# Kernel optimization log

Hardware: AMD Instinct MI355X
Metric: run time of the kernel (lower is better)

Reference implementation:

```python
import jax
import jax.numpy as jnp
from jax import lax
import numpy as np

B, T, D = 64, 256, 512      # batch, seq_len, input_size
H, P, L = 1024, 256, 4      # hidden_size, proj_size, num_layers


def setup_inputs() -> dict:
    key = jax.random.key(0)
    ks = jax.random.split(key, 12)
    s = 1.0 / np.sqrt(H)
    inp = {
        "x": jax.random.normal(ks[0], (B, T, D), dtype=jnp.float32),
        # layer 0 (input dim D)
        "W_ih0": jax.random.uniform(ks[1], (4 * H, D), minval=-s, maxval=s, dtype=jnp.float32),
        "W_hh0": jax.random.uniform(ks[2], (4 * H, P), minval=-s, maxval=s, dtype=jnp.float32),
        "b_ih0": jax.random.uniform(ks[3], (4 * H,), minval=-s, maxval=s, dtype=jnp.float32),
        "b_hh0": jax.random.uniform(ks[4], (4 * H,), minval=-s, maxval=s, dtype=jnp.float32),
        "W_hr0": jax.random.uniform(ks[5], (P, H), minval=-s, maxval=s, dtype=jnp.float32),
        # layers 1..L-1 (input dim P), stacked
        "W_ihs": jax.random.uniform(ks[6], (L - 1, 4 * H, P), minval=-s, maxval=s, dtype=jnp.float32),
        "W_hhs": jax.random.uniform(ks[7], (L - 1, 4 * H, P), minval=-s, maxval=s, dtype=jnp.float32),
        "b_ihs": jax.random.uniform(ks[8], (L - 1, 4 * H), minval=-s, maxval=s, dtype=jnp.float32),
        "b_hhs": jax.random.uniform(ks[9], (L - 1, 4 * H), minval=-s, maxval=s, dtype=jnp.float32),
        "W_hrs": jax.random.uniform(ks[10], (L - 1, P, H), minval=-s, maxval=s, dtype=jnp.float32),
    }
    return inp


def _lstm_proj_layer(x, W_ih, W_hh, b_ih, b_hh, W_hr):
    """One projected-LSTM layer (PyTorch gate order i,f,g,o). x: [B,T,Din] -> [B,T,P]."""
    b, t, _ = x.shape
    p, h = W_hr.shape
    # precompute input contribution to gates: [T,B,4H]
    xg = jnp.swapaxes(jnp.einsum('btd,gd->btg', x, W_ih) + b_ih + b_hh, 0, 1)

    def step(carry, g_in):
        hp, c = carry                      # hp: [B,P] projected hidden, c: [B,H]
        g = g_in + hp @ W_hh.T             # [B,4H]
        i, f, gg, o = jnp.split(g, 4, axis=-1)
        i = jax.nn.sigmoid(i)
        f = jax.nn.sigmoid(f)
        gg = jnp.tanh(gg)
        o = jax.nn.sigmoid(o)
        c = f * c + i * gg
        hp = (o * jnp.tanh(c)) @ W_hr.T    # projection: [B,P]
        return (hp, c), hp

    init = (jnp.zeros((b, p), x.dtype), jnp.zeros((b, h), x.dtype))
    _, hs = lax.scan(step, init, xg)       # hs: [T,B,P]
    return jnp.swapaxes(hs, 0, 1)


def reference(x, W_ih0, W_hh0, b_ih0, b_hh0, W_hr0, W_ihs, W_hhs, b_ihs, b_hhs, W_hrs):
    y = _lstm_proj_layer(x, W_ih0, W_hh0, b_ih0, b_hh0, W_hr0)
    for l in range(L - 1):  # fixed small layer count
        y = _lstm_proj_layer(y, W_ihs[l], W_hhs[l], b_ihs[l], b_hhs[l], W_hrs[l])
    return y[:, -1, :]  # [B, P] last-timestep output, as in forward()
```

## Files before the change

kernel.cpp:

```cpp
#include <hip/hip_runtime.h>
#include <cstdint>
#include <cstddef>


#define B_ 64
#define T_ 256
#define D_ 512
#define H_ 1024
#define P_ 256
#define NWG 256
#define NTHR 512

using short8  = __attribute__((ext_vector_type(8))) short;
using f32x16  = __attribute__((ext_vector_type(16))) float;
using f32x4   = __attribute__((ext_vector_type(4))) float;

__device__ inline float bf2f(short s) {
  unsigned u = ((unsigned)(unsigned short)s) << 16;
  return __builtin_bit_cast(float, u);
}
__device__ inline unsigned short f2bf(float f) {
  unsigned u = __builtin_bit_cast(unsigned, f);
  u += 0x7fffu + ((u >> 16) & 1u);
  return (unsigned short)(u >> 16);
}
__device__ inline void split1(float v, short& hi, short& lo) {
  unsigned short h = f2bf(v);
  hi = (short)h;
  lo = (short)f2bf(v - bf2f((short)h));
}
__device__ inline unsigned packf(float v) {
  short h, l;
  split1(v, h, l);
  return (unsigned)(unsigned short)h | ((unsigned)(unsigned short)l << 16);
}
__device__ inline void split8(const float* p, short8& hi, short8& lo) {
  float4 a = *(const float4*)p;
  float4 b = *(const float4*)(p + 4);
  float v[8] = {a.x, a.y, a.z, a.w, b.x, b.y, b.z, b.w};
#pragma unroll
  for (int i = 0; i < 8; ++i) {
    short h, l;
    split1(v[i], h, l);
    hi[i] = h; lo[i] = l;
  }
}
__device__ inline void unpack_c8(const unsigned* p, short8& hi, short8& lo) {
  uint4 a = *(const uint4*)p;
  uint4 b = *(const uint4*)(p + 4);
  unsigned w[8] = {a.x, a.y, a.z, a.w, b.x, b.y, b.z, b.w};
#pragma unroll
  for (int i = 0; i < 8; ++i) {
    hi[i] = (short)(w[i] & 0xffff);
    lo[i] = (short)(w[i] >> 16);
  }
}
__device__ inline void unpack_a8(const unsigned* p, short8& hi, short8& lo) {
#pragma unroll
  for (int i = 0; i < 4; ++i) {
    unsigned long long v = __hip_atomic_load((const unsigned long long*)p + i,
                                             __ATOMIC_RELAXED, __HIP_MEMORY_SCOPE_AGENT);
    unsigned w0 = (unsigned)v, w1 = (unsigned)(v >> 32);
    hi[2 * i]     = (short)(w0 & 0xffff);
    lo[2 * i]     = (short)(w0 >> 16);
    hi[2 * i + 1] = (short)(w1 & 0xffff);
    lo[2 * i + 1] = (short)(w1 >> 16);
  }
}
__device__ inline float sigm(float x)   { return 1.f / (1.f + __expf(-x)); }
__device__ inline float tanh_f(float x) { return 1.f - 2.f / (__expf(2.f * x) + 1.f); }

#define NCNT 32
#define REL_IDX 768
__device__ inline void gbar(unsigned* cnt, unsigned ep) {
  __syncthreads();
  if (blockIdx.x == 0) {
    if (threadIdx.x < 64) {
      if (threadIdx.x == 0)
        __hip_atomic_fetch_add(&cnt[0], 1u, __ATOMIC_RELAXED,
                               __HIP_MEMORY_SCOPE_AGENT);
      const unsigned tgt = ep * (NWG / NCNT);
      for (;;) {
        unsigned v = tgt;
        if (threadIdx.x < NCNT)
          v = __hip_atomic_load(&cnt[threadIdx.x * 16], __ATOMIC_RELAXED,
                                __HIP_MEMORY_SCOPE_AGENT);
        if (__all(v >= tgt)) break;
        __builtin_amdgcn_s_sleep(2);
      }
      if (threadIdx.x == 0)
        __hip_atomic_store(&cnt[REL_IDX], ep, __ATOMIC_RELAXED,
                           __HIP_MEMORY_SCOPE_AGENT);
    }
  } else {
    if (threadIdx.x == 0) {
      __hip_atomic_fetch_add(&cnt[(blockIdx.x & (NCNT - 1)) * 16], 1u,
                             __ATOMIC_RELAXED, __HIP_MEMORY_SCOPE_AGENT);
      while (__hip_atomic_load(&cnt[REL_IDX], __ATOMIC_RELAXED,
                               __HIP_MEMORY_SCOPE_AGENT) < ep)
        __builtin_amdgcn_s_sleep(2);
    }
  }
  __syncthreads();
}

#define WP_W0I 0
#define WP_W0H 2097152
#define WP_WIS 3145728
#define WP_WHS 6291456
#define WP_WR  9437184
#define WP_CHUNKS 1310720

template <bool PK>
__global__ __launch_bounds__(NTHR) void lstm_kernel(
    const float* __restrict__ x,
    const float* __restrict__ Wih0, const float* __restrict__ Whh0,
    const float* __restrict__ bih0, const float* __restrict__ bhh0,
    const float* __restrict__ Whr0,
    const float* __restrict__ Wihs, const float* __restrict__ Whhs,
    const float* __restrict__ bihs, const float* __restrict__ bhhs,
    const float* __restrict__ Whrs,
    float* __restrict__ out,
    unsigned* __restrict__ yR, unsigned* __restrict__ hR,
    unsigned* __restrict__ WP, unsigned* __restrict__ cnt)
{
  __shared__ float sGA[64 * 64];
  __shared__ float sGB[64 * 64];
  __shared__ float sBias[64];
  __shared__ float sRed[8 * 64 * 4];

  const int tid  = threadIdx.x;
  const int wg   = blockIdx.x;
  const int lane = tid & 63;
  const int wave = tid >> 6;
  const int bh   = wave & 1;
  const int kq   = wave >> 1;
  const int lg   = wg >> 6;
  const int wgl  = wg & 63;

  const int m1  = bh * 32 + (lane & 31);
  const int n1  = lane & 31;
  const int kh1 = (lane >> 5) * 8;

  const float* Wih = (lg == 0) ? Wih0 : Wihs + (size_t)(lg - 1) * 4096 * 256;
  const float* Whh = (lg == 0) ? Whh0 : Whhs + (size_t)(lg - 1) * 4096 * 256;
  const float* bih = (lg == 0) ? bih0 : bihs + (size_t)(lg - 1) * 4096;
  const float* bhh = (lg == 0) ? bhh0 : bhhs + (size_t)(lg - 1) * 4096;
  const float* Whr = (lg == 0) ? Whr0 : Whrs + (size_t)(lg - 1) * 256 * 1024;
  const unsigned* WPI = (lg == 0) ? WP + WP_W0I
                                  : WP + WP_WIS + (size_t)(lg - 1) * 1048576;
  const unsigned* WPH = (lg == 0) ? WP + WP_W0H
                                  : WP + WP_WHS + (size_t)(lg - 1) * 1048576;
  const unsigned* WPR = WP + WP_WR + (size_t)lg * 262144;

  unsigned* hP = hR + (size_t)lg * (B_ * H_);

  unsigned ep = 0;
  if (PK) {
    for (int c = wg * NTHR + tid; c < WP_CHUNKS; c += NWG * NTHR) {
      const float* src; unsigned* dst;
      int c0 = c;
      if (c0 < 262144) {
        src = Wih0 + (size_t)c0 * 8;  dst = WP + WP_W0I + (size_t)c0 * 8;
      } else if ((c0 -= 262144) < 131072) {
        src = Whh0 + (size_t)c0 * 8;  dst = WP + WP_W0H + (size_t)c0 * 8;
      } else if ((c0 -= 131072) < 393216) {
        src = Wihs + (size_t)c0 * 8;  dst = WP + WP_WIS + (size_t)c0 * 8;
      } else if ((c0 -= 393216) < 393216) {
        src = Whhs + (size_t)c0 * 8;  dst = WP + WP_WHS + (size_t)c0 * 8;
      } else {
        c0 -= 393216;
        src = (c0 < 32768) ? (Whr0 + (size_t)c0 * 8)
                           : (Whrs + (size_t)(c0 - 32768) * 8);
        dst = WP + WP_WR + (size_t)c0 * 8;
      }
      unsigned u[8];
#pragma unroll
      for (int i = 0; i < 8; ++i) u[i] = packf(src[i]);
#pragma unroll
      for (int i = 0; i < 4; ++i) {
        unsigned long long q = (unsigned long long)u[2 * i] |
                               ((unsigned long long)u[2 * i + 1] << 32);
        __hip_atomic_store((unsigned long long*)dst + i, q,
                           __ATOMIC_RELAXED, __HIP_MEMORY_SCOPE_AGENT);
      }
    }
  }
  ep++; gbar(cnt, ep);
  __threadfence();

  if (tid < 64) {
    int c = tid;
    int R = (c & 3) * H_ + wgl * 16 + (c >> 2);
    sBias[c] = bih[R] + bhh[R];
  }
  __syncthreads();

  float cs[2];
  cs[0] = 0.f; cs[1] = 0.f;

  const int R0 = (n1 & 3) * H_ + wgl * 16 + (n1 >> 2);

  for (int tick = 0; tick < T_ + 3; ++tick) {
    const int t = tick - lg;
    const bool act = (t >= 0) && (t < T_);

    if (act) {
      f32x16 aH[2] = {{}, {}};
      f32x16 aL[2] = {{}, {}};
      f32x16 aM[2] = {{}, {}};

      if (lg == 0) {
        const float* ax = x + ((size_t)m1 * T_ + t) * D_ + kh1;
#pragma unroll 2
        for (int k0 = kq * 128; k0 < kq * 128 + 128; k0 += 16) {
          short8 Ah, Al;
          split8(ax + k0, Ah, Al);
#pragma unroll
          for (int T = 0; T < 2; ++T) {
            short8 Bh, Bl;
            const size_t off = (size_t)(R0 + T * 8) * D_ + kh1 + k0;
            if (PK) unpack_c8(WPI + off, Bh, Bl);
            else    split8(Wih + off, Bh, Bl);
            aH[T] = __builtin_amdgcn_mfma_f32_32x32x16_bf16(Ah, Bh, aH[T], 0, 0, 0);
            aL[T] = __builtin_amdgcn_mfma_f32_32x32x16_bf16(Ah, Bl, aL[T], 0, 0, 0);
            aM[T] = __builtin_amdgcn_mfma_f32_32x32x16_bf16(Al, Bh, aM[T], 0, 0, 0);
          }
        }
      } else {
        const unsigned* ay = yR + (size_t)((lg - 1) * 2 + (t & 1)) * (B_ * P_)
                             + (size_t)m1 * P_ + kh1;
#pragma unroll 2
        for (int k0 = kq * 64; k0 < kq * 64 + 64; k0 += 16) {
          short8 Ah, Al;
          unpack_a8(ay + k0, Ah, Al);
#pragma unroll
          for (int T = 0; T < 2; ++T) {
            short8 Bh, Bl;
            const size_t off = (size_t)(R0 + T * 8) * P_ + kh1 + k0;
            if (PK) unpack_c8(WPI + off, Bh, Bl);
            else    split8(Wih + off, Bh, Bl);
            aH[T] = __builtin_amdgcn_mfma_f32_32x32x16_bf16(Ah, Bh, aH[T], 0, 0, 0);
            aL[T] = __builtin_amdgcn_mfma_f32_32x32x16_bf16(Ah, Bl, aL[T], 0, 0, 0);
            aM[T] = __builtin_amdgcn_mfma_f32_32x32x16_bf16(Al, Bh, aM[T], 0, 0, 0);
          }
        }
      }
      if (t > 0) {
        const unsigned* ay = yR + (size_t)(lg * 2 + ((t - 1) & 1)) * (B_ * P_)
                             + (size_t)m1 * P_ + kh1;
#pragma unroll 2
        for (int k0 = kq * 64; k0 < kq * 64 + 64; k0 += 16) {
          short8 Ah, Al;
          unpack_a8(ay + k0, Ah, Al);
#pragma unroll
          for (int T = 0; T < 2; ++T) {
            short8 Bh, Bl;
            const size_t off = (size_t)(R0 + T * 8) * P_ + kh1 + k0;
            if (PK) unpack_c8(WPH + off, Bh, Bl);
            else    split8(Whh + off, Bh, Bl);
            aH[T] = __builtin_amdgcn_mfma_f32_32x32x16_bf16(Ah, Bh, aH[T], 0, 0, 0);
            aL[T] = __builtin_amdgcn_mfma_f32_32x32x16_bf16(Ah, Bl, aL[T], 0, 0, 0);
            aM[T] = __builtin_amdgcn_mfma_f32_32x32x16_bf16(Al, Bh, aM[T], 0, 0, 0);
          }
        }
      }
      {
        float* sgc = (kq >= 2) ? sGB : sGA;
        if ((kq & 1) == 0) {
#pragma unroll
          for (int T = 0; T < 2; ++T)
#pragma unroll
            for (int r = 0; r < 16; ++r) {
              int mrow = (r & 3) + 8 * (r >> 2) + 4 * (lane >> 5) + bh * 32;
              sgc[mrow * 64 + T * 32 + n1] = aH[T][r] + aL[T][r] + aM[T][r];
            }
        }
        __syncthreads();
        if ((kq & 1) == 1) {
#pragma unroll
          for (int T = 0; T < 2; ++T)
#pragma unroll
            for (int r = 0; r < 16; ++r) {
              int mrow = (r & 3) + 8 * (r >> 2) + 4 * (lane >> 5) + bh * 32;
              sgc[mrow * 64 + T * 32 + n1] += aH[T][r] + aL[T][r] + aM[T][r];
            }
        }
        __syncthreads();
      }
      {
        const int b  = tid >> 3;
        const int ub = (tid & 7) * 2;
        const float* gA = &sGA[b * 64];
        const float* gB = &sGB[b * 64];
        unsigned pw[2];
#pragma unroll
        for (int j = 0; j < 2; ++j) {
          int cb = (ub + j) * 4;
          float ii = sigm(gA[cb + 0] + gB[cb + 0] + sBias[cb + 0]);
          float ff = sigm(gA[cb + 1] + gB[cb + 1] + sBias[cb + 1]);
          float gg = tanh_f(gA[cb + 2] + gB[cb + 2] + sBias[cb + 2]);
          float oo = sigm(gA[cb + 3] + gB[cb + 3] + sBias[cb + 3]);
          float cv = ff * cs[j] + ii * gg;
          cs[j] = cv;
          pw[j] = packf(oo * tanh_f(cv));
        }
        size_t ho = (size_t)b * H_ + wgl * 16 + ub;
        unsigned long long q0 = (unsigned long long)pw[0] |
                                ((unsigned long long)pw[1] << 32);
        __hip_atomic_store((unsigned long long*)&hP[ho], q0,
                           __ATOMIC_RELAXED, __HIP_MEMORY_SCOPE_AGENT);
      }
    }
    ep++; gbar(cnt, ep);

    if (act) {
      const int mt0  = (wgl >> 4) * 16;
      const int p0   = (wgl & 15) * 16;
      const int l16  = lane & 15;
      const int kh2  = (lane >> 4) * 8 + wave * 128;
      const unsigned* ahp = hP + (size_t)(mt0 + l16) * H_ + kh2;
      f32x4 q0 = {}, q1 = {}, q2 = {};
      if (PK) {
        const unsigned* wb = WPR + (size_t)(p0 + l16) * H_ + kh2;
#pragma unroll 2
        for (int k0 = 0; k0 < 128; k0 += 32) {
          short8 Ah, Al, Bh, Bl;
          unpack_a8(ahp + k0, Ah, Al);
          unpack_c8(wb + k0, Bh, Bl);
          q0 = __builtin_amdgcn_mfma_f32_16x16x32_bf16(Ah, Bh, q0, 0, 0, 0);
          q1 = __builtin_amdgcn_mfma_f32_16x16x32_bf16(Ah, Bl, q1, 0, 0, 0);
          q2 = __builtin_amdgcn_mfma_f32_16x16x32_bf16(Al, Bh, q2, 0, 0, 0);
        }
      } else {
        const float* wf = Whr + (size_t)(p0 + l16) * H_ + kh2;
#pragma unroll 2
        for (int k0 = 0; k0 < 128; k0 += 32) {
          short8 Ah, Al, Bh, Bl;
          unpack_a8(ahp + k0, Ah, Al);
          split8(wf + k0, Bh, Bl);
          q0 = __builtin_amdgcn_mfma_f32_16x16x32_bf16(Ah, Bh, q0, 0, 0, 0);
          q1 = __builtin_amdgcn_mfma_f32_16x16x32_bf16(Ah, Bl, q1, 0, 0, 0);
          q2 = __builtin_amdgcn_mfma_f32_16x16x32_bf16(Al, Bh, q2, 0, 0, 0);
        }
      }
      f32x4 a4;
#pragma unroll
      for (int r = 0; r < 4; ++r) a4[r] = q0[r] + q1[r] + q2[r];
      *(f32x4*)&sRed[(wave * 64 + lane) * 4] = a4;
      __syncthreads();
      if (wave == 0) {
        float v4[4];
#pragma unroll
        for (int r = 0; r < 4; ++r) v4[r] = a4[r];
#pragma unroll
        for (int w = 1; w < 8; ++w) {
          f32x4 pw = *(const f32x4*)&sRed[(w * 64 + lane) * 4];
#pragma unroll
          for (int r = 0; r < 4; ++r) v4[r] += pw[r];
        }
        unsigned* yo = yR + (size_t)(lg * 2 + (t & 1)) * (B_ * P_);
#pragma unroll
        for (int r = 0; r < 4; ++r) {
          int mm = mt0 + (lane >> 4) * 4 + r;
          __hip_atomic_store(&yo[(size_t)mm * P_ + p0 + l16], packf(v4[r]),
                             __ATOMIC_RELAXED, __HIP_MEMORY_SCOPE_AGENT);
          if (lg == 3 && t == T_ - 1) out[mm * P_ + p0 + l16] = v4[r];
        }
      }
    }
    ep++; gbar(cnt, ep);
  }
}

extern "C" void kernel_launch(void* const* d_in, const int* in_sizes, int n_in,
                              void* d_out, int out_size, void* d_ws, size_t ws_size,
                              hipStream_t stream) {
  const float* x    = (const float*)d_in[0];
  const float* Wih0 = (const float*)d_in[1];
  const float* Whh0 = (const float*)d_in[2];
  const float* bih0 = (const float*)d_in[3];
  const float* bhh0 = (const float*)d_in[4];
  const float* Whr0 = (const float*)d_in[5];
  const float* Wihs = (const float*)d_in[6];
  const float* Whhs = (const float*)d_in[7];
  const float* bihs = (const float*)d_in[8];
  const float* bhhs = (const float*)d_in[9];
  const float* Whrs = (const float*)d_in[10];
  float* out = (float*)d_out;

  char* ws = (char*)d_ws;
  unsigned* cnt = (unsigned*)ws;
  unsigned* hR  = (unsigned*)(ws + 4096);
  unsigned* yR  = (unsigned*)(ws + 4096 + 1048576);
  unsigned* WP  = (unsigned*)(ws + 1576960);
  const size_t need_pk = 1576960ull + 41943040ull;
  const bool pk = (ws_size >= need_pk);

  (void)hipMemsetAsync(d_ws, 0, 4096, stream);

  void* args[] = {&x, &Wih0, &Whh0, &bih0, &bhh0, &Whr0,
                  &Wihs, &Whhs, &bihs, &bhhs, &Whrs,
                  &out, &yR, &hR, &WP, &cnt};
  hipError_t st;
  if (pk) {
    auto* kfn = lstm_kernel<true>;
    st = hipLaunchCooperativeKernel((void*)kfn, dim3(NWG), dim3(NTHR),
                                    args, 0, stream);
    if (st != hipSuccess)
      lstm_kernel<true><<<dim3(NWG), dim3(NTHR), 0, stream>>>(
          x, Wih0, Whh0, bih0, bhh0, Whr0, Wihs, Whhs, bihs, bhhs, Whrs,
          out, yR, hR, WP, cnt);
  } else {
    auto* kfn = lstm_kernel<false>;
    st = hipLaunchCooperativeKernel((void*)kfn, dim3(NWG), dim3(NTHR),
                                    args, 0, stream);
    if (st != hipSuccess)
      lstm_kernel<false><<<dim3(NWG), dim3(NTHR), 0, stream>>>(
          x, Wih0, Whh0, bih0, bhh0, Whr0, Wihs, Whhs, bihs, bhhs, Whrs,
          out, yR, hR, WP, cnt);
  }
}
```

Baseline: 8.119 ms.

## Pin recurrent weights in LDS/registers and batch layer-0 input GEMM over four timesteps

Each workgroup now keeps its packed W_hh slice (and W_ih for layers 1-3) in shared memory and its W_hr slice in registers, so the per-step loop no longer re-reads these weights from global memory. Layer 0's input projection is computed four timesteps at a time into a per-workgroup global ring buffer, reusing each weight load across four x rows. The per-step gate reduction now goes through a single shared buffer in four serialized passes. This costs more LDS, which may limit occupancy, and adds extra syncs plus ring traffic on layer 0, which could make layer 0 the slowest stage of the pipeline.

```diff
diff --git a/kernel.cpp b/kernel.cpp
--- a/kernel.cpp
+++ b/kernel.cpp
@@ -10,6 +10,7 @@
 #define P_ 256
 #define NWG 256
 #define NTHR 512
+#define WST 260
 
 using short8  = __attribute__((ext_vector_type(8))) short;
 using f32x16  = __attribute__((ext_vector_type(16))) float;
@@ -111,7 +112,7 @@
 #define WP_WR  9437184
 #define WP_CHUNKS 1310720
 
-template <bool PK>
+template <bool PIN>
 __global__ __launch_bounds__(NTHR) void lstm_kernel(
     const float* __restrict__ x,
     const float* __restrict__ Wih0, const float* __restrict__ Whh0,
@@ -122,12 +123,16 @@
     const float* __restrict__ Whrs,
     float* __restrict__ out,
     unsigned* __restrict__ yR, unsigned* __restrict__ hR,
-    unsigned* __restrict__ WP, unsigned* __restrict__ cnt)
+    unsigned* __restrict__ WP, float* __restrict__ gI,
+    unsigned* __restrict__ cnt)
 {
-  __shared__ float sGA[64 * 64];
-  __shared__ float sGB[64 * 64];
+  __shared__ unsigned sWI[PIN ? 64 * WST : 1];
+  __shared__ unsigned sWH[PIN ? 64 * WST : 1];
+  __shared__ float sG [PIN ? 64 * 64 : 1];
+  __shared__ float sGA[PIN ? 1 : 64 * 64];
+  __shared__ float sGB[PIN ? 1 : 64 * 64];
+  __shared__ float sRed[8 * 64 * 4];
   __shared__ float sBias[64];
-  __shared__ float sRed[8 * 64 * 4];
 
   const int tid  = threadIdx.x;
   const int wg   = blockIdx.x;
@@ -154,9 +159,10 @@
   const unsigned* WPR = WP + WP_WR + (size_t)lg * 262144;
 
   unsigned* hP = hR + (size_t)lg * (B_ * H_);
+  float*    myRing = gI + (size_t)wgl * 32768;
 
   unsigned ep = 0;
-  if (PK) {
+  if (PIN) {
     for (int c = wg * NTHR + tid; c < WP_CHUNKS; c += NWG * NTHR) {
       const float* src; unsigned* dst;
       int c0 = c;
@@ -194,12 +200,86 @@
     int R = (c & 3) * H_ + wgl * 16 + (c >> 2);
     sBias[c] = bih[R] + bhh[R];
   }
+
+  if (PIN) {
+    if (lg > 0) {
+      for (int idx = tid; idx < 64 * 32; idx += NTHR) {
+        int s = idx >> 5, c = (idx & 31) * 8;
+        int R = ((s & 31) & 3) * H_ + wgl * 16 + ((s & 31) >> 2) + (s >> 5) * 8;
+        const unsigned* src = WPI + (size_t)R * 256 + c;
+        uint4 a = *(const uint4*)src, b = *(const uint4*)(src + 4);
+        *(uint4*)&sWI[s * WST + c] = a;
+        *(uint4*)&sWI[s * WST + c + 4] = b;
+      }
+    }
+    for (int idx = tid; idx < 64 * 32; idx += NTHR) {
+      int s = idx >> 5, c = (idx & 31) * 8;
+      int R = ((s & 31) & 3) * H_ + wgl * 16 + ((s & 31) >> 2) + (s >> 5) * 8;
+      const unsigned* src = WPH + (size_t)R * 256 + c;
+      uint4 a = *(const uint4*)src, b = *(const uint4*)(src + 4);
+      *(uint4*)&sWH[s * WST + c] = a;
+      *(uint4*)&sWH[s * WST + c + 4] = b;
+    }
+  }
   __syncthreads();
+
+  unsigned wr[32];
+  const int l16p = lane & 15;
+  const int kh2p = (lane >> 4) * 8 + wave * 128;
+  if (PIN) {
+    const unsigned* wb = WPR + (size_t)((wgl & 15) * 16 + l16p) * 1024 + kh2p;
+#pragma unroll
+    for (int k = 0; k < 4; ++k)
+#pragma unroll
+      for (int j = 0; j < 8; ++j) wr[k * 8 + j] = wb[k * 32 + j];
+  }
+
+  const int R0 = (n1 & 3) * H_ + wgl * 16 + (n1 >> 2);
+
+  auto group_in = [&](int tg) {
+    f32x16 ac[2][4] = {{{}, {}, {}, {}}, {{}, {}, {}, {}}};
+    for (int k0 = kq * 128; k0 < kq * 128 + 128; k0 += 16) {
+      short8 B0h, B0l, B1h, B1l;
+      unpack_c8(WPI + (size_t)R0 * 512 + kh1 + k0, B0h, B0l);
+      unpack_c8(WPI + (size_t)(R0 + 8) * 512 + kh1 + k0, B1h, B1l);
+#pragma unroll
+      for (int st = 0; st < 4; ++st) {
+        short8 Ah, Al;
+        split8(x + ((size_t)m1 * T_ + tg + st) * D_ + kh1 + k0, Ah, Al);
+        ac[0][st] = __builtin_amdgcn_mfma_f32_32x32x16_bf16(Ah, B0h, ac[0][st], 0, 0, 0);
+        ac[0][st] = __builtin_amdgcn_mfma_f32_32x32x16_bf16(Ah, B0l, ac[0][st], 0, 0, 0);
+        ac[0][st] = __builtin_amdgcn_mfma_f32_32x32x16_bf16(Al, B0h, ac[0][st], 0, 0, 0);
+        ac[1][st] = __builtin_amdgcn_mfma_f32_32x32x16_bf16(Ah, B1h, ac[1][st], 0, 0, 0);
+        ac[1][st] = __builtin_amdgcn_mfma_f32_32x32x16_bf16(Ah, B1l, ac[1][st], 0, 0, 0);
+        ac[1][st] = __builtin_amdgcn_mfma_f32_32x32x16_bf16(Al, B1h, ac[1][st], 0, 0, 0);
+      }
+    }
+#pragma unroll
+    for (int st = 0; st < 4; ++st) {
+#pragma unroll
+      for (int step = 0; step < 4; ++step) {
+        if (kq == step) {
+#pragma unroll
+          for (int T = 0; T < 2; ++T)
+#pragma unroll
+            for (int r = 0; r < 16; ++r) {
+              int mrow = (r & 3) + 8 * (r >> 2) + 4 * (lane >> 5) + bh * 32;
+              if (step == 0) sG[mrow * 64 + T * 32 + n1]  = ac[T][st][r];
+              else           sG[mrow * 64 + T * 32 + n1] += ac[T][st][r];
+            }
+        }
+        __syncthreads();
+      }
+      float* ring = myRing + ((tg + st) & 7) * 4096;
+      for (int i = tid; i < 1024; i += NTHR)
+        ((float4*)ring)[i] = ((const float4*)sG)[i];
+      __syncthreads();
+    }
+  };
+  if (PIN && lg == 0) group_in(0);
 
   float cs[2];
   cs[0] = 0.f; cs[1] = 0.f;
-
-  const int R0 = (n1 & 3) * H_ + wgl * 16 + (n1 >> 2);
 
   for (int tick = 0; tick < T_ + 3; ++tick) {
     const int t = tick - lg;
@@ -210,106 +290,178 @@
       f32x16 aL[2] = {{}, {}};
       f32x16 aM[2] = {{}, {}};
 
-      if (lg == 0) {
-        const float* ax = x + ((size_t)m1 * T_ + t) * D_ + kh1;
+      if (PIN) {
+        if (lg > 0) {
+          const unsigned* ay = yR + (size_t)((lg - 1) * 2 + (t & 1)) * (B_ * P_)
+                               + (size_t)m1 * P_ + kh1;
 #pragma unroll 2
-        for (int k0 = kq * 128; k0 < kq * 128 + 128; k0 += 16) {
-          short8 Ah, Al;
-          split8(ax + k0, Ah, Al);
-#pragma unroll
-          for (int T = 0; T < 2; ++T) {
-            short8 Bh, Bl;
-            const size_t off = (size_t)(R0 + T * 8) * D_ + kh1 + k0;
-            if (PK) unpack_c8(WPI + off, Bh, Bl);
-            else    split8(Wih + off, Bh, Bl);
-            aH[T] = __builtin_amdgcn_mfma_f32_32x32x16_bf16(Ah, Bh, aH[T], 0, 0, 0);
-            aL[T] = __builtin_amdgcn_mfma_f32_32x32x16_bf16(Ah, Bl, aL[T], 0, 0, 0);
-            aM[T] = __builtin_amdgcn_mfma_f32_32x32x16_bf16(Al, Bh, aM[T], 0, 0, 0);
-          }
+          for (int k0 = kq * 64; k0 < kq * 64 + 64; k0 += 16) {
+            short8 Ah, Al;
+            unpack_a8(ay + k0, Ah, Al);
+#pragma unroll
+            for (int T = 0; T < 2; ++T) {
+              short8 Bh, Bl;
+              unpack_c8(&sWI[(T * 32 + n1) * WST + kh1 + k0], Bh, Bl);
+              aH[T] = __builtin_amdgcn_mfma_f32_32x32x16_bf16(Ah, Bh, aH[T], 0, 0, 0);
+              aL[T] = __builtin_amdgcn_mfma_f32_32x32x16_bf16(Ah, Bl, aL[T], 0, 0, 0);
+              aM[T] = __builtin_amdgcn_mfma_f32_32x32x16_bf16(Al, Bh, aM[T], 0, 0, 0);
+            }
+          }
+        }
+        if (t > 0) {
+          const unsigned* ay = yR + (size_t)(lg * 2 + ((t - 1) & 1)) * (B_ * P_)
+                               + (size_t)m1 * P_ + kh1;
+#pragma unroll 2
+          for (int k0 = kq * 64; k0 < kq * 64 + 64; k0 += 16) {
+            short8 Ah, Al;
+            unpack_a8(ay + k0, Ah, Al);
+#pragma unroll
+            for (int T = 0; T < 2; ++T) {
+              short8 Bh, Bl;
+              unpack_c8(&sWH[(T * 32 + n1) * WST + kh1 + k0], Bh, Bl);
+              aH[T] = __builtin_amdgcn_mfma_f32_32x32x16_bf16(Ah, Bh, aH[T], 0, 0, 0);
+              aL[T] = __builtin_amdgcn_mfma_f32_32x32x16_bf16(Ah, Bl, aL[T], 0, 0, 0);
+              aM[T] = __builtin_amdgcn_mfma_f32_32x32x16_bf16(Al, Bh, aM[T], 0, 0, 0);
+            }
+          }
+        }
+#pragma unroll
+        for (int step = 0; step < 4; ++step) {
+          if (kq == step) {
+#pragma unroll
+            for (int T = 0; T < 2; ++T)
+#pragma unroll
+              for (int r = 0; r < 16; ++r) {
+                int mrow = (r & 3) + 8 * (r >> 2) + 4 * (lane >> 5) + bh * 32;
+                float v = aH[T][r] + aL[T][r] + aM[T][r];
+                if (step == 0) sG[mrow * 64 + T * 32 + n1]  = v;
+                else           sG[mrow * 64 + T * 32 + n1] += v;
+              }
+          }
+          __syncthreads();
+        }
+        {
+          const int b  = tid >> 3;
+          const int ub = (tid & 7) * 2;
+          const float* gp = &sG[b * 64];
+          const float* rp = myRing + (t & 7) * 4096 + b * 64;
+          unsigned pw[2];
+#pragma unroll
+          for (int j = 0; j < 2; ++j) {
+            int cb = (ub + j) * 4;
+            float g0 = gp[cb + 0], g1 = gp[cb + 1], g2 = gp[cb + 2], g3 = gp[cb + 3];
+            if (lg == 0) { g0 += rp[cb + 0]; g1 += rp[cb + 1];
+                           g2 += rp[cb + 2]; g3 += rp[cb + 3]; }
+            float ii = sigm(g0 + sBias[cb + 0]);
+            float ff = sigm(g1 + sBias[cb + 1]);
+            float gg = tanh_f(g2 + sBias[cb + 2]);
+            float oo = sigm(g3 + sBias[cb + 3]);
+            float cv = ff * cs[j] + ii * gg;
+            cs[j] = cv;
+            pw[j] = packf(oo * tanh_f(cv));
+          }
+          size_t ho = (size_t)(tid >> 3) * H_ + wgl * 16 + ub;
+          unsigned long long q0 = (unsigned long long)pw[0] |
+                                  ((unsigned long long)pw[1] << 32);
+          __hip_atomic_store((unsigned long long*)&hP[ho], q0,
+                             __ATOMIC_RELAXED, __HIP_MEMORY_SCOPE_AGENT);
         }
       } else {
-        const unsigned* ay = yR + (size_t)((lg - 1) * 2 + (t & 1)) * (B_ * P_)
-                             + (size_t)m1 * P_ + kh1;
+        if (lg == 0) {
+          const float* ax = x + ((size_t)m1 * T_ + t) * D_ + kh1;
 #pragma unroll 2
-        for (int k0 = kq * 64; k0 < kq * 64 + 64; k0 += 16) {
-          short8 Ah, Al;
-          unpack_a8(ay + k0, Ah, Al);
-#pragma unroll
-          for (int T = 0; T < 2; ++T) {
-            short8 Bh, Bl;
-            const size_t off = (size_t)(R0 + T * 8) * P_ + kh1 + k0;
-            if (PK) unpack_c8(WPI + off, Bh, Bl);
-            else    split8(Wih + off, Bh, Bl);
-            aH[T] = __builtin_amdgcn_mfma_f32_32x32x16_bf16(Ah, Bh, aH[T], 0, 0, 0);
-            aL[T] = __builtin_amdgcn_mfma_f32_32x32x16_bf16(Ah, Bl, aL[T], 0, 0, 0);
-            aM[T] = __builtin_amdgcn_mfma_f32_32x32x16_bf16(Al, Bh, aM[T], 0, 0, 0);
-          }
-        }
-      }
-      if (t > 0) {
-        const unsigned* ay = yR + (size_t)(lg * 2 + ((t - 1) & 1)) * (B_ * P_)
-                             + (size_t)m1 * P_ + kh1;
+          for (int k0 = kq * 128; k0 < kq * 128 + 128; k0 += 16) {
+            short8 Ah, Al;
+            split8(ax + k0, Ah, Al);
+#pragma unroll
+            for (int T = 0; T < 2; ++T) {
+              short8 Bh, Bl;
+              split8(Wih + (size_t)(R0 + T * 8) * D_ + kh1 + k0, Bh, Bl);
+              aH[T] = __builtin_amdgcn_mfma_f32_32x32x16_bf16(Ah, Bh, aH[T], 0, 0, 0);
+              aL[T] = __builtin_amdgcn_mfma_f32_32x32x16_bf16(Ah, Bl, aL[T], 0, 0, 0);
+              aM[T] = __builtin_amdgcn_mfma_f32_32x32x16_bf16(Al, Bh, aM[T], 0, 0, 0);
+            }
+          }
+        } else {
+          const unsigned* ay = yR + (size_t)((lg - 1) * 2 + (t & 1)) * (B_ * P_)
+                               + (size_t)m1 * P_ + kh1;
 #pragma unroll 2
-        for (int k0 = kq * 64; k0 < kq * 64 + 64; k0 += 16) {
-          short8 Ah, Al;
-          unpack_a8(ay + k0, Ah, Al);
-#pragma unroll
-          for (int T = 0; T < 2; ++T) {
-            short8 Bh, Bl;
-            const size_t off = (size_t)(R0 + T * 8) * P_ + kh1 + k0;
-            if (PK) unpack_c8(WPH + off, Bh, Bl);
-            else    split8(Whh + off, Bh, Bl);
-            aH[T] = __builtin_amdgcn_mfma_f32_32x32x16_bf16(Ah, Bh, aH[T], 0, 0, 0);
-            aL[T] = __builtin_amdgcn_mfma_f32_32x32x16_bf16(Ah, Bl, aL[T], 0, 0, 0);
-            aM[T] = __builtin_amdgcn_mfma_f32_32x32x16_bf16(Al, Bh, aM[T], 0, 0, 0);
-          }
-        }
-      }
-      {
-        float* sgc = (kq >= 2) ? sGB : sGA;
-        if ((kq & 1) == 0) {
-#pragma unroll
-          for (int T = 0; T < 2; ++T)
-#pragma unroll
-            for (int r = 0; r < 16; ++r) {
-              int mrow = (r & 3) + 8 * (r >> 2) + 4 * (lane >> 5) + bh * 32;
-              sgc[mrow * 64 + T * 32 + n1] = aH[T][r] + aL[T][r] + aM[T][r];
+          for (int k0 = kq * 64; k0 < kq * 64 + 64; k0 += 16) {
+            short8 Ah, Al;
+            unpack_a8(ay + k0, Ah, Al);
+#pragma unroll
+            for (int T = 0; T < 2; ++T) {
+              short8 Bh, Bl;
+              split8(Wih + (size_t)(R0 + T * 8) * P_ + kh1 + k0, Bh, Bl);
+              aH[T] = __builtin_amdgcn_mfma_f32_32x32x16_bf16(Ah, Bh, aH[T], 0, 0, 0);
+              aL[T] = __builtin_amdgcn_mfma_f32_32x32x16_bf16(Ah, Bl, aL[T], 0, 0, 0);
+              aM[T] = __builtin_amdgcn_mfma_f32_32x32x16_bf16(Al, Bh, aM[T], 0, 0, 0);
             }
-        }
-        __syncthreads();
-        if ((kq & 1) == 1) {
-#pragma unroll
-          for (int T = 0; T < 2; ++T)
-#pragma unroll
-            for (int r = 0; r < 16; ++r) {
-              int mrow = (r & 3) + 8 * (r >> 2) + 4 * (lane >> 5) + bh * 32;
-              sgc[mrow * 64 + T * 32 + n1] += aH[T][r] + aL[T][r] + aM[T][r];
+          }
+        }
+        if (t > 0) {
+          const unsigned* ay = yR + (size_t)(lg * 2 + ((t - 1) & 1)) * (B_ * P_)
+                               + (size_t)m1 * P_ + kh1;
+#pragma unroll 2
+          for (int k0 = kq * 64; k0 < kq * 64 + 64; k0 += 16) {
+            short8 Ah, Al;
+            unpack_a8(ay + k0, Ah, Al);
+#pragma unroll
+            for (int T = 0; T < 2; ++T) {
+              short8 Bh, Bl;
+              split8(Whh + (size_t)(R0 + T * 8) * P_ + kh1 + k0, Bh, Bl);
+              aH[T] = __builtin_amdgcn_mfma_f32_32x32x16_bf16(Ah, Bh, aH[T], 0, 0, 0);
+              aL[T] = __builtin_amdgcn_mfma_f32_32x32x16_bf16(Ah, Bl, aL[T], 0, 0, 0);
+              aM[T] = __builtin_amdgcn_mfma_f32_32x32x16_bf16(Al, Bh, aM[T], 0, 0, 0);
             }
-        }
-        __syncthreads();
-      }
-      {
-        const int b  = tid >> 3;
-        const int ub = (tid & 7) * 2;
-        const float* gA = &sGA[b * 64];
-        const float* gB = &sGB[b * 64];
-        unsigned pw[2];
-#pragma unroll
-        for (int j = 0; j < 2; ++j) {
-          int cb = (ub + j) * 4;
-          float ii = sigm(gA[cb + 0] + gB[cb + 0] + sBias[cb + 0]);
-          float ff = sigm(gA[cb + 1] + gB[cb + 1] + sBias[cb + 1]);
-          float gg = tanh_f(gA[cb + 2] + gB[cb + 2] + sBias[cb + 2]);
-          float oo = sigm(gA[cb + 3] + gB[cb + 3] + sBias[cb + 3]);
-          float cv = ff * cs[j] + ii * gg;
-          cs[j] = cv;
-          pw[j] = packf(oo * tanh_f(cv));
-        }
-        size_t ho = (size_t)b * H_ + wgl * 16 + ub;
-        unsigned long long q0 = (unsigned long long)pw[0] |
-                                ((unsigned long long)pw[1] << 32);
-        __hip_atomic_store((unsigned long long*)&hP[ho], q0,
-                           __ATOMIC_RELAXED, __HIP_MEMORY_SCOPE_AGENT);
+          }
+        }
+        {
+          float* sgc = (kq >= 2) ? sGB : sGA;
+          if ((kq & 1) == 0) {
+#pragma unroll
+            for (int T = 0; T < 2; ++T)
+#pragma unroll
+              for (int r = 0; r < 16; ++r) {
+                int mrow = (r & 3) + 8 * (r >> 2) + 4 * (lane >> 5) + bh * 32;
+                sgc[mrow * 64 + T * 32 + n1] = aH[T][r] + aL[T][r] + aM[T][r];
+              }
+          }
+          __syncthreads();
+          if ((kq & 1) == 1) {
+#pragma unroll
+            for (int T = 0; T < 2; ++T)
+#pragma unroll
+              for (int r = 0; r < 16; ++r) {
+                int mrow = (r & 3) + 8 * (r >> 2) + 4 * (lane >> 5) + bh * 32;
+                sgc[mrow * 64 + T * 32 + n1] += aH[T][r] + aL[T][r] + aM[T][r];
+              }
+          }
+          __syncthreads();
+        }
+        {
+          const int b  = tid >> 3;
+          const int ub = (tid & 7) * 2;
+          const float* gA = &sGA[b * 64];
+          const float* gB = &sGB[b * 64];
+          unsigned pw[2];
+#pragma unroll
+          for (int j = 0; j < 2; ++j) {
+            int cb = (ub + j) * 4;
+            float ii = sigm(gA[cb + 0] + gB[cb + 0] + sBias[cb + 0]);
+            float ff = sigm(gA[cb + 1] + gB[cb + 1] + sBias[cb + 1]);
+            float gg = tanh_f(gA[cb + 2] + gB[cb + 2] + sBias[cb + 2]);
+            float oo = sigm(gA[cb + 3] + gB[cb + 3] + sBias[cb + 3]);
+            float cv = ff * cs[j] + ii * gg;
+            cs[j] = cv;
+            pw[j] = packf(oo * tanh_f(cv));
+          }
+          size_t ho = (size_t)b * H_ + wgl * 16 + ub;
+          unsigned long long q0 = (unsigned long long)pw[0] |
+                                  ((unsigned long long)pw[1] << 32);
+          __hip_atomic_store((unsigned long long*)&hP[ho], q0,
+                             __ATOMIC_RELAXED, __HIP_MEMORY_SCOPE_AGENT);
+        }
       }
     }
     ep++; gbar(cnt, ep);
@@ -317,23 +469,24 @@
     if (act) {
       const int mt0  = (wgl >> 4) * 16;
       const int p0   = (wgl & 15) * 16;
-      const int l16  = lane & 15;
-      const int kh2  = (lane >> 4) * 8 + wave * 128;
-      const unsigned* ahp = hP + (size_t)(mt0 + l16) * H_ + kh2;
+      const unsigned* ahp = hP + (size_t)(mt0 + l16p) * H_ + kh2p;
       f32x4 q0 = {}, q1 = {}, q2 = {};
-      if (PK) {
-        const unsigned* wb = WPR + (size_t)(p0 + l16) * H_ + kh2;
-#pragma unroll 2
-        for (int k0 = 0; k0 < 128; k0 += 32) {
+      if (PIN) {
+#pragma unroll
+        for (int k = 0; k < 4; ++k) {
           short8 Ah, Al, Bh, Bl;
-          unpack_a8(ahp + k0, Ah, Al);
-          unpack_c8(wb + k0, Bh, Bl);
+          unpack_a8(ahp + k * 32, Ah, Al);
+#pragma unroll
+          for (int j = 0; j < 8; ++j) {
+            Bh[j] = (short)(wr[k * 8 + j] & 0xffff);
+            Bl[j] = (short)(wr[k * 8 + j] >> 16);
+          }
           q0 = __builtin_amdgcn_mfma_f32_16x16x32_bf16(Ah, Bh, q0, 0, 0, 0);
           q1 = __builtin_amdgcn_mfma_f32_16x16x32_bf16(Ah, Bl, q1, 0, 0, 0);
           q2 = __builtin_amdgcn_mfma_f32_16x16x32_bf16(Al, Bh, q2, 0, 0, 0);
         }
       } else {
-        const float* wf = Whr + (size_t)(p0 + l16) * H_ + kh2;
+        const float* wf = Whr + (size_t)(p0 + l16p) * H_ + kh2p;
 #pragma unroll 2
         for (int k0 = 0; k0 < 128; k0 += 32) {
           short8 Ah, Al, Bh, Bl;
@@ -363,11 +516,12 @@
 #pragma unroll
         for (int r = 0; r < 4; ++r) {
           int mm = mt0 + (lane >> 4) * 4 + r;
-          __hip_atomic_store(&yo[(size_t)mm * P_ + p0 + l16], packf(v4[r]),
+          __hip_atomic_store(&yo[(size_t)mm * P_ + p0 + l16p], packf(v4[r]),
                              __ATOMIC_RELAXED, __HIP_MEMORY_SCOPE_AGENT);
-          if (lg == 3 && t == T_ - 1) out[mm * P_ + p0 + l16] = v4[r];
-        }
-      }
+          if (lg == 3 && t == T_ - 1) out[mm * P_ + p0 + l16p] = v4[r];
+        }
+      }
+      if (PIN && lg == 0 && (t & 3) == 3 && t + 1 < T_) group_in(t + 1);
     }
     ep++; gbar(cnt, ep);
   }
@@ -392,25 +546,26 @@
   char* ws = (char*)d_ws;
   unsigned* cnt = (unsigned*)ws;
   unsigned* hR  = (unsigned*)(ws + 4096);
-  unsigned* yR  = (unsigned*)(ws + 4096 + 1048576);
-  unsigned* WP  = (unsigned*)(ws + 1576960);
-  const size_t need_pk = 1576960ull + 41943040ull;
-  const bool pk = (ws_size >= need_pk);
+  unsigned* yR  = (unsigned*)(ws + 1052672);
+  float*    gI  = (float*)(ws + 1576960);
+  unsigned* WP  = (unsigned*)(ws + 9965568);
+  const size_t need_pin = 9965568ull + 41943040ull;
+  const bool pin = (ws_size >= need_pin);
 
   (void)hipMemsetAsync(d_ws, 0, 4096, stream);
 
   void* args[] = {&x, &Wih0, &Whh0, &bih0, &bhh0, &Whr0,
                   &Wihs, &Whhs, &bihs, &bhhs, &Whrs,
-                  &out, &yR, &hR, &WP, &cnt};
+                  &out, &yR, &hR, &WP, &gI, &cnt};
   hipError_t st;
-  if (pk) {
+  if (pin) {
     auto* kfn = lstm_kernel<true>;
     st = hipLaunchCooperativeKernel((void*)kfn, dim3(NWG), dim3(NTHR),
                                     args, 0, stream);
     if (st != hipSuccess)
       lstm_kernel<true><<<dim3(NWG), dim3(NTHR), 0, stream>>>(
           x, Wih0, Whh0, bih0, bhh0, Whr0, Wihs, Whhs, bihs, bhhs, Whrs,
-          out, yR, hR, WP, cnt);
+          out, yR, hR, WP, gI, cnt);
   } else {
     auto* kfn = lstm_kernel<false>;
     st = hipLaunchCooperativeKernel((void*)kfn, dim3(NWG), dim3(NTHR),
@@ -418,6 +573,6 @@
     if (st != hipSuccess)
       lstm_kernel<false><<<dim3(NWG), dim3(NTHR), 0, stream>>>(
           x, Wih0, Whh0, bih0, bhh0, Whr0, Wihs, Whhs, bihs, bhhs, Whrs,
-          out, yR, hR, WP, cnt);
-  }
-}
+          out, yR, hR, WP, gI, cnt);
+  }
+}
```

Result: faster. 7.252 ms (-10.7%).
